# Optimization experiments

Hardware: AMD Instinct MI355X
Metric: run time of the kernel (lower is better)

The kernel has to match this reference:

```python
import jax, jax.numpy as jnp
import numpy as np
import math

H, W = 180, 320          # frame_shape
RF = 16                  # rf_diameter
K = 20
T = 400                  # video frames
FRAME_RATE = 120.0
ALPHA, BETA, GAMMA = 50.0, 1.0, 0.0   # soft-rectifier params
CENTER_SIGMA, SURROUND_SIGMA = 4.0, 8.0
CENTER_STR, SURROUND_STR = 1.0, -0.8
COVERAGE = 0.5


def _mosaic():
    # hexagonal lattice of cell centers (replicates _tile_cells)
    s = CENTER_SIGMA / COVERAGE
    B = np.array([[s, s / 2.0], [0.0, s * math.sqrt(3.0) / 2.0]], dtype=np.float64)
    Binv = np.linalg.inv(B)
    margin = CENTER_SIGMA / 2.0
    corners = np.array([[0, 0], [W, 0], [0, H], [W, H]], dtype=np.float64)
    lc = corners @ Binv.T
    n0, n1 = int(np.floor(lc[:, 0].min())) - 1, int(np.ceil(lc[:, 0].max())) + 1
    m0, m1 = int(np.floor(lc[:, 1].min())) - 1, int(np.ceil(lc[:, 1].max())) + 1
    pos = []
    for m in range(m0, m1 + 1):
        for n in range(n0, n1 + 1):
            p = np.array([float(n), float(m)]) @ B.T
            if margin <= p[0] <= W - margin and margin <= p[1] <= H - margin:
                pos.append((p[0], p[1]))
    return np.array(pos, dtype=np.float32)


def _rf_indices(mosaic):
    # flat pixel indices into the (H+2RF, W+2RF) zero-padded frame
    pw = W + 2 * RF
    yy, xx = np.meshgrid(np.arange(RF), np.arange(RF), indexing='ij')
    local = (yy * pw + xx).ravel()
    out = []
    for x0, y0 in mosaic:
        v = math.floor(y0 - RF / 2.0) + RF
        h = math.floor(x0 - RF / 2.0) + RF
        out.append(local + v * pw + h)
    return np.stack(out).astype(np.int32)


def _filter():
    # DoG spatial filter
    c = RF / 2.0
    yy, xx = np.meshgrid(np.arange(RF, dtype=np.float32), np.arange(RF, dtype=np.float32), indexing='ij')
    d2 = (xx - c) ** 2 + (yy - c) ** 2
    cen = np.exp(-d2 / (2 * CENTER_SIGMA ** 2)); cen /= cen.sum()
    sur = np.exp(-d2 / (2 * SURROUND_SIGMA ** 2)); sur /= sur.sum()
    spatial = CENTER_STR * cen + SURROUND_STR * sur
    # biphasic temporal filter with smooth onset, ON cell, flipped
    dt = 1000.0 / FRAME_RATE
    t = np.arange(K, dtype=np.float32) * dt
    l1 = 1.0 * np.exp(-(t - 40.0) ** 2 / (2 * 20.0 ** 2))
    l2 = 0.6 * np.exp(-(t - 100.0) ** 2 / (2 * 40.0 ** 2))
    onset = 1.0 - np.exp(-t / 15.0)
    temporal = ((l1 - l2) * onset)[::-1].copy()
    st = temporal[:, None, None] * spatial[None]
    st = st / np.linalg.norm(st)
    return st.reshape(-1).astype(np.float32)


def setup_inputs() -> dict:
    key = jax.random.key(0)
    x = jax.random.normal(key, (T, H, W), dtype=jnp.float32)
    mosaic = _mosaic()
    return {
        'x': x,
        'w': jnp.asarray(_filter()),                    # (K*RF*RF,)
        'rf_indices': jnp.asarray(_rf_indices(mosaic)),  # (N_cells, RF*RF)
    }


def reference(x, w, rf_indices):
    # x: (T,H,W); w: (K*RF*RF,); rf_indices: (N, RF*RF) int32
    xp = jnp.pad(x, ((0, 0), (RF, RF), (RF, RF)))
    flat = xp.reshape(x.shape[0], -1)              # (T, (H+2RF)*(W+2RF))
    patches = jnp.take(flat, rf_indices, axis=1)   # (T, N, RF*RF) irregular gather
    wk = w.reshape(K, RF * RF)
    # spatial projection against each temporal tap
    y = jnp.einsum('tnp,kp->tnk', patches, wk)     # (T, N, K)
    n_win = x.shape[0] - K + 1
    # generator[i, n] = sum_k y[i+k, n, k]  (sliding-window spatiotemporal dot)
    g = y[0:n_win, :, 0]
    for k in range(1, K):
        g = g + y[k:k + n_win, :, k]
    out = ALPHA * jax.nn.softplus(BETA * (g - GAMMA))  # soft-rectifier nonlinearity
    return out.T                                    # (N_cells, n_windows)
```

## Files before the change

kernel.cpp:

```cpp
#include <hip/hip_runtime.h>
#include <math.h>

constexpr int H_ = 180, W_ = 320, RF_ = 16, K_ = 20, T_ = 400;
constexpr int HW_ = H_ * W_;
constexpr int NWIN = T_ - K_ + 1;
constexpr int PW   = W_ + 2 * RF_;
constexpr float ALPHA = 50.0f, BETA = 1.0f, GAMMA = 0.0f;
constexpr int NXCD = 8;
constexpr int T_PER_XCD = T_ / NXCD;
constexpr int CH = 8;

template <int CTRL>
__device__ inline float dpp_add(float v) {
    int s = __builtin_amdgcn_update_dpp(0, __float_as_int(v), CTRL, 0xF, 0xF, true);
    return v + __int_as_float(s);
}
__device__ inline float swz_xor4_add(float v) {
    return v + __int_as_float(
        __builtin_amdgcn_ds_swizzle(__float_as_int(v), 0x101F));
}

#if __has_builtin(__builtin_amdgcn_permlane32_swap)
__device__ inline float pl32_merge(float a, float b) {
    auto r = __builtin_amdgcn_permlane32_swap(
        __float_as_uint(a), __float_as_uint(b), false, false);
    return __uint_as_float(r[0]) + __uint_as_float(r[1]);
}
#else
__device__ inline float pl32_merge(float a, float b) {
    bool hi = (threadIdx.x & 32) != 0;
    float keep = hi ? b : a, send = hi ? a : b;
    return keep + __shfl_xor(send, 32, 64);
}
#endif

#if __has_builtin(__builtin_amdgcn_permlane16_swap)
__device__ inline float pl16_merge(float a, float b) {
    auto r = __builtin_amdgcn_permlane16_swap(
        __float_as_uint(a), __float_as_uint(b), false, false);
    return __uint_as_float(r[0]) + __uint_as_float(r[1]);
}
#else
__device__ inline float pl16_merge(float a, float b) {
    bool hi = (threadIdx.x & 16) != 0;
    float keep = hi ? b : a, send = hi ? a : b;
    return keep + __shfl_xor(send, 16, 64);
}
#endif

__device__ inline float allred64(float v) {
    v = dpp_add<0xB1>(v);
    v = dpp_add<0x4E>(v);
    v = swz_xor4_add(v);
    v = dpp_add<0x128>(v);
    v = pl16_merge(v, v);
    v = pl32_merge(v, v);
    return v;
}

__global__ __launch_bounds__(512) void prep_kernel(
    const float* __restrict__ w,
    float* __restrict__ spatial, float* __restrict__ temporal)
{
    __shared__ float ss_l[32];
    int tid = threadIdx.x;
    int wv  = tid >> 6;
    int l   = tid & 63;

    for (int k = wv; k < K_; k += 8) {
        float s = 0.0f;
#pragma unroll
        for (int j = 0; j < 4; ++j) {
            float v = w[k * 256 + l + j * 64];
            s = fmaf(v, v, s);
        }
        s = allred64(s);
        if (l == 0) ss_l[k] = s;
    }
    __syncthreads();

    float best = -1.0f;
    int k0 = 0;
    for (int k = 0; k < K_; ++k) {
        float v = ss_l[k];
        if (v > best) { best = v; k0 = k; }
    }

    for (int k = wv; k < K_; k += 8) {
        float d = 0.0f;
#pragma unroll
        for (int j = 0; j < 4; ++j)
            d = fmaf(w[k * 256 + l + j * 64], w[k0 * 256 + l + j * 64], d);
        d = allred64(d);
        if (l == 0) temporal[k] = d / best;
    }
    if (tid < 256) spatial[tid] = w[k0 * 256 + tid];
}

__global__ __launch_bounds__(256) void stage1_kernel(
    const float* __restrict__ x, const int* __restrict__ rf,
    const float* __restrict__ spatial, float* __restrict__ y,
    int N)
{
    int lane = threadIdx.x & 63;
    int wid  = threadIdx.x >> 6;

    int b   = blockIdx.x;
    int xcd = b & (NXCD - 1);
    int nch = b >> 3;

    int n = nch * 4 + wid;
    if (n >= N) return;
    int t0 = xcd * T_PER_XCD;

    int base = rf[n * 256];
    int r0 = base / PW - RF_;
    int c0 = base % PW - RF_;
    int r0c = min(max(r0, 0), H_ - RF_);
    int c0c = min(max(c0, 0), W_ - RF_);

    int lr = lane >> 2;
    int q  = lane & 3;
    int off = (r0c + lr) * W_ + c0c + q * 4;

    float wv[4];
    int rr = lr + (r0c - r0);
#pragma unroll
    for (int j = 0; j < 4; ++j) {
        int cc = q * 4 + j + (c0c - c0);
        bool ok = (rr >= 0) & (rr < RF_) & (cc >= 0) & (cc < RF_);
        wv[j] = ok ? spatial[rr * RF_ + cc] : 0.0f;
    }

    const float* xp = x + (size_t)t0 * HW_ + off;
    float* yp = y + (size_t)n * T_ + t0;

    bool b8 = (lane & 8) != 0;

    for (int tt = 0; tt < 48; tt += CH) {
        float4 buf[CH];
#pragma unroll
        for (int j = 0; j < CH; ++j)
            buf[j] = *reinterpret_cast<const float4*>(xp + (size_t)(tt + j) * HW_);

        float acc[CH];
#pragma unroll
        for (int j = 0; j < CH; ++j) {
            float a = buf[j].x * wv[0];
            a = fmaf(buf[j].y, wv[1], a);
            a = fmaf(buf[j].z, wv[2], a);
            acc[j] = fmaf(buf[j].w, wv[3], a);
        }

        float m0 = pl32_merge(acc[0], acc[4]);
        float m1 = pl32_merge(acc[1], acc[5]);
        float m2 = pl32_merge(acc[2], acc[6]);
        float m3 = pl32_merge(acc[3], acc[7]);
        float n0 = pl16_merge(m0, m2);
        float n1 = pl16_merge(m1, m3);
        float c0v = dpp_add<0x128>(n0);
        float c1v = dpp_add<0x128>(n1);
        float C = b8 ? c1v : c0v;
        C = dpp_add<0xB1>(C);
        C = dpp_add<0x4E>(C);
        C = swz_xor4_add(C);

        if ((lane & 7) == 0)
            yp[tt + (lane >> 3)] = C;
    }

#pragma unroll
    for (int f = 48; f < T_PER_XCD; ++f) {
        float4 v = *reinterpret_cast<const float4*>(xp + (size_t)f * HW_);
        float a = v.x * wv[0];
        a = fmaf(v.y, wv[1], a);
        a = fmaf(v.z, wv[2], a);
        a = fmaf(v.w, wv[3], a);
        a = allred64(a);
        if (lane == 0) yp[f] = a;
    }
}

__global__ void stage2_kernel(const float* __restrict__ y,
                              const float* __restrict__ temporal,
                              float* __restrict__ out, int N)
{
    __shared__ float tw[K_];
    if (threadIdx.x < K_) tw[threadIdx.x] = temporal[threadIdx.x];
    __syncthreads();

    int n  = blockIdx.x;
    int t0 = threadIdx.x;
    if (n >= N || t0 >= NWIN) return;

    const float* yn = y + (size_t)n * T_;
    float g = 0.0f;
#pragma unroll
    for (int k = 0; k < K_; ++k)
        g = fmaf(yn[t0 + k], tw[k], g);

    float z = BETA * (g - GAMMA);
    float sp = fmaxf(z, 0.0f) + log1pf(expf(-fabsf(z)));
    out[n * NWIN + t0] = ALPHA * sp;
}

extern "C" void kernel_launch(void* const* d_in, const int* in_sizes, int n_in,
                              void* d_out, int out_size, void* d_ws, size_t ws_size,
                              hipStream_t stream)
{
    const float* x  = (const float*)d_in[0];
    const float* w  = (const float*)d_in[1];
    const int*   rf = (const int*)d_in[2];

    int N   = in_sizes[2] / (RF_ * RF_);
    int NCH = (N + 3) / 4;

    float* spatial  = (float*)d_ws;
    float* temporal = spatial + 256;
    float* y        = spatial + 512;

    prep_kernel<<<1, 512, 0, stream>>>(w, spatial, temporal);
    stage1_kernel<<<NXCD * NCH, 256, 0, stream>>>(x, rf, spatial, y, N);
    stage2_kernel<<<N, 384, 0, stream>>>(y, temporal, (float*)d_out, N);
}
```

Before: 45.01 us.

## Stage frame bands into LDS and compute all cells per band from shared tiles

New measurement: 57.37 us. +27.5%, slower.

```diff
diff --git a/kernel.cpp b/kernel.cpp
--- a/kernel.cpp
+++ b/kernel.cpp
@@ -6,9 +6,17 @@
 constexpr int NWIN = T_ - K_ + 1;
 constexpr int PW   = W_ + 2 * RF_;
 constexpr float ALPHA = 50.0f, BETA = 1.0f, GAMMA = 0.0f;
-constexpr int NXCD = 8;
-constexpr int T_PER_XCD = T_ / NXCD;
-constexpr int CH = 8;
+
+constexpr int BSTEP  = 28;
+constexpr int NBANDS = 6;
+constexpr int BROWS  = 43;
+constexpr int RP     = 328;
+constexpr int CHUNKS = (BROWS * RP + 255) / 256;
+constexpr int BUFW   = CHUNKS * 256;
+constexpr int WPR = 36, WROWS = 32;
+constexpr int LDSW_W = WROWS * WPR;
+constexpr int CF = 10;
+constexpr int NCHUNKS_T = T_ / CF;
 
 template <int CTRL>
 __device__ inline float dpp_add(float v) {
@@ -19,7 +27,6 @@
     return v + __int_as_float(
         __builtin_amdgcn_ds_swizzle(__float_as_int(v), 0x101F));
 }
-
 #if __has_builtin(__builtin_amdgcn_permlane32_swap)
 __device__ inline float pl32_merge(float a, float b) {
     auto r = __builtin_amdgcn_permlane32_swap(
@@ -33,7 +40,6 @@
     return keep + __shfl_xor(send, 32, 64);
 }
 #endif
-
 #if __has_builtin(__builtin_amdgcn_permlane16_swap)
 __device__ inline float pl16_merge(float a, float b) {
     auto r = __builtin_amdgcn_permlane16_swap(
@@ -47,7 +53,6 @@
     return keep + __shfl_xor(send, 16, 64);
 }
 #endif
-
 __device__ inline float allred64(float v) {
     v = dpp_add<0xB1>(v);
     v = dpp_add<0x4E>(v);
@@ -57,127 +62,147 @@
     v = pl32_merge(v, v);
     return v;
 }
-
-__global__ __launch_bounds__(512) void prep_kernel(
-    const float* __restrict__ w,
-    float* __restrict__ spatial, float* __restrict__ temporal)
-{
-    __shared__ float ss_l[32];
-    int tid = threadIdx.x;
-    int wv  = tid >> 6;
-    int l   = tid & 63;
-
-    for (int k = wv; k < K_; k += 8) {
-        float s = 0.0f;
-#pragma unroll
-        for (int j = 0; j < 4; ++j) {
-            float v = w[k * 256 + l + j * 64];
-            s = fmaf(v, v, s);
-        }
-        s = allred64(s);
-        if (l == 0) ss_l[k] = s;
+__device__ inline float red16(float v) {
+    v = dpp_add<0xB1>(v);
+    v = dpp_add<0x4E>(v);
+    v = swz_xor4_add(v);
+    v = dpp_add<0x128>(v);
+    return v;
+}
+
+__global__ __launch_bounds__(1024) void prep_kernel(
+    const float* __restrict__ w, const int* __restrict__ rf,
+    float* __restrict__ temporal, float* __restrict__ spat_pad,
+    int* __restrict__ cnt, int4* __restrict__ lists, int N)
+{
+    __shared__ float ss[32];
+    int tid = threadIdx.x, wv = tid >> 6, l = tid & 63;
+    if (tid < NBANDS) cnt[tid] = 0;
+    __syncthreads();
+
+    if (wv < 8) {
+        for (int k = wv; k < K_; k += 8) {
+            float s = 0.0f;
+#pragma unroll
+            for (int j = 0; j < 4; ++j) {
+                float v = w[k * 256 + l + j * 64];
+                s = fmaf(v, v, s);
+            }
+            s = allred64(s);
+            if (l == 0) ss[k] = s;
+        }
+    } else {
+        for (int n = tid - 512; n < N; n += 512) {
+            int base = rf[n * 256];
+            int v0 = base / PW;
+            int r0 = v0 - RF_;
+            int c0 = (base - v0 * PW) - RF_;
+            int r0c = min(max(r0, 0), H_ - RF_);
+            int c0c = min(max(c0, 0), W_ - RF_);
+            int b = r0c / BSTEP;
+            int slot = atomicAdd(&cnt[b], 1);
+            int4 d;
+            d.x = n;
+            d.y = (r0c - b * BSTEP) * RP + c0c;
+            d.z = (r0c - r0 + 8) * WPR + (c0c - c0 + 8);
+            d.w = 0;
+            lists[b * N + slot] = d;
+        }
     }
     __syncthreads();
 
     float best = -1.0f;
     int k0 = 0;
     for (int k = 0; k < K_; ++k) {
-        float v = ss_l[k];
+        float v = ss[k];
         if (v > best) { best = v; k0 = k; }
     }
 
-    for (int k = wv; k < K_; k += 8) {
-        float d = 0.0f;
-#pragma unroll
-        for (int j = 0; j < 4; ++j)
-            d = fmaf(w[k * 256 + l + j * 64], w[k0 * 256 + l + j * 64], d);
-        d = allred64(d);
-        if (l == 0) temporal[k] = d / best;
-    }
-    if (tid < 256) spatial[tid] = w[k0 * 256 + tid];
-}
-
-__global__ __launch_bounds__(256) void stage1_kernel(
-    const float* __restrict__ x, const int* __restrict__ rf,
-    const float* __restrict__ spatial, float* __restrict__ y,
-    int N)
-{
-    int lane = threadIdx.x & 63;
-    int wid  = threadIdx.x >> 6;
-
-    int b   = blockIdx.x;
-    int xcd = b & (NXCD - 1);
-    int nch = b >> 3;
-
-    int n = nch * 4 + wid;
-    if (n >= N) return;
-    int t0 = xcd * T_PER_XCD;
-
-    int base = rf[n * 256];
-    int r0 = base / PW - RF_;
-    int c0 = base % PW - RF_;
-    int r0c = min(max(r0, 0), H_ - RF_);
-    int c0c = min(max(c0, 0), W_ - RF_);
-
-    int lr = lane >> 2;
-    int q  = lane & 3;
-    int off = (r0c + lr) * W_ + c0c + q * 4;
-
-    float wv[4];
-    int rr = lr + (r0c - r0);
-#pragma unroll
-    for (int j = 0; j < 4; ++j) {
-        int cc = q * 4 + j + (c0c - c0);
+    if (wv < 8) {
+        for (int k = wv; k < K_; k += 8) {
+            float d = 0.0f;
+#pragma unroll
+            for (int j = 0; j < 4; ++j)
+                d = fmaf(w[k * 256 + l + j * 64], w[k0 * 256 + l + j * 64], d);
+            d = allred64(d);
+            if (l == 0) temporal[k] = d / best;
+        }
+    }
+    for (int i = tid; i < LDSW_W; i += 1024) {
+        int rr = i / WPR - 8;
+        int cc = i % WPR - 8;
         bool ok = (rr >= 0) & (rr < RF_) & (cc >= 0) & (cc < RF_);
-        wv[j] = ok ? spatial[rr * RF_ + cc] : 0.0f;
-    }
-
-    const float* xp = x + (size_t)t0 * HW_ + off;
-    float* yp = y + (size_t)n * T_ + t0;
-
-    bool b8 = (lane & 8) != 0;
-
-    for (int tt = 0; tt < 48; tt += CH) {
-        float4 buf[CH];
-#pragma unroll
-        for (int j = 0; j < CH; ++j)
-            buf[j] = *reinterpret_cast<const float4*>(xp + (size_t)(tt + j) * HW_);
-
-        float acc[CH];
-#pragma unroll
-        for (int j = 0; j < CH; ++j) {
-            float a = buf[j].x * wv[0];
-            a = fmaf(buf[j].y, wv[1], a);
-            a = fmaf(buf[j].z, wv[2], a);
-            acc[j] = fmaf(buf[j].w, wv[3], a);
-        }
-
-        float m0 = pl32_merge(acc[0], acc[4]);
-        float m1 = pl32_merge(acc[1], acc[5]);
-        float m2 = pl32_merge(acc[2], acc[6]);
-        float m3 = pl32_merge(acc[3], acc[7]);
-        float n0 = pl16_merge(m0, m2);
-        float n1 = pl16_merge(m1, m3);
-        float c0v = dpp_add<0x128>(n0);
-        float c1v = dpp_add<0x128>(n1);
-        float C = b8 ? c1v : c0v;
-        C = dpp_add<0xB1>(C);
-        C = dpp_add<0x4E>(C);
-        C = swz_xor4_add(C);
-
-        if ((lane & 7) == 0)
-            yp[tt + (lane >> 3)] = C;
-    }
-
-#pragma unroll
-    for (int f = 48; f < T_PER_XCD; ++f) {
-        float4 v = *reinterpret_cast<const float4*>(xp + (size_t)f * HW_);
-        float a = v.x * wv[0];
-        a = fmaf(v.y, wv[1], a);
-        a = fmaf(v.z, wv[2], a);
-        a = fmaf(v.w, wv[3], a);
-        a = allred64(a);
-        if (lane == 0) yp[f] = a;
+        spat_pad[i] = ok ? w[k0 * 256 + rr * RF_ + cc] : 0.0f;
+    }
+}
+
+__global__ __launch_bounds__(1024) void stage1_kernel(
+    const float* __restrict__ x, const float* __restrict__ spat_pad,
+    const int* __restrict__ cnt, const int4* __restrict__ lists,
+    float* __restrict__ y, int N)
+{
+    __shared__ float lds[2 * BUFW + LDSW_W];
+    float* ldsw = lds + 2 * BUFW;
+
+    int tid  = threadIdx.x;
+    int wv   = tid >> 6;
+    int lane = tid & 63;
+
+    int b       = blockIdx.x % NBANDS;
+    int chunkid = blockIdx.x / NBANDS;
+    int f0      = chunkid * CF;
+    int band0   = b * BSTEP;
+
+    for (int i = tid; i < LDSW_W; i += 1024) ldsw[i] = spat_pad[i];
+
+    int count = cnt[b];
+    const int4* list = lists + (size_t)b * N;
+    int g = lane >> 4;
+    int r = lane & 15;
+
+    auto stage = [&](int sel, int f) {
+        const float* xf = x + (size_t)f * HW_;
+        for (int ck = wv; ck < CHUNKS; ck += 16) {
+            int w0  = ck * 256 + lane * 4;
+            int row = w0 / RP;
+            int col = w0 - row * RP;
+            int srow = min(band0 + row, H_ - 1);
+            int scol = min(col, W_ - 4);
+            const float* gp = xf + srow * W_ + scol;
+            __builtin_amdgcn_global_load_lds(
+                (const __attribute__((address_space(1))) void*)gp,
+                (__attribute__((address_space(3))) void*)(lds + sel * BUFW + ck * 256),
+                16, 0, 0);
+        }
+    };
+
+    auto compute = [&](int sel, int t) {
+        const float* buf = lds + sel * BUFW;
+        for (int i = wv * 4 + g; i < count; i += 64) {
+            int4 d = list[i];
+            int ax = d.y + r * RP;
+            int aw = d.z + r * WPR;
+            float a = 0.0f;
+#pragma unroll
+            for (int q = 0; q < 4; ++q) {
+                float4 pv = *reinterpret_cast<const float4*>(buf + ax + q * 4);
+                float4 wq = *reinterpret_cast<const float4*>(ldsw + aw + q * 4);
+                a = fmaf(pv.x, wq.x, a);
+                a = fmaf(pv.y, wq.y, a);
+                a = fmaf(pv.z, wq.z, a);
+                a = fmaf(pv.w, wq.w, a);
+            }
+            a = red16(a);
+            if (r == 0) y[(size_t)d.x * T_ + t] = a;
+        }
+    };
+
+    stage(0, f0);
+    __syncthreads();
+    for (int j = 0; j < CF; ++j) {
+        if (j + 1 < CF) stage((j + 1) & 1, f0 + j + 1);
+        compute(j & 1, f0 + j);
+        __syncthreads();
     }
 }
 
@@ -212,14 +237,15 @@
     const float* w  = (const float*)d_in[1];
     const int*   rf = (const int*)d_in[2];
 
-    int N   = in_sizes[2] / (RF_ * RF_);
-    int NCH = (N + 3) / 4;
-
-    float* spatial  = (float*)d_ws;
-    float* temporal = spatial + 256;
-    float* y        = spatial + 512;
-
-    prep_kernel<<<1, 512, 0, stream>>>(w, spatial, temporal);
-    stage1_kernel<<<NXCD * NCH, 256, 0, stream>>>(x, rf, spatial, y, N);
+    int N = in_sizes[2] / (RF_ * RF_);
+
+    float* temporal = (float*)d_ws;
+    int*   cnt      = (int*)d_ws + 64;
+    float* spat_pad = (float*)d_ws + 128;
+    int4*  lists    = (int4*)((int*)d_ws + 1280);
+    float* y        = (float*)d_ws + 1280 + 4 * NBANDS * N;
+
+    prep_kernel<<<1, 1024, 0, stream>>>(w, rf, temporal, spat_pad, cnt, lists, N);
+    stage1_kernel<<<NCHUNKS_T * NBANDS, 1024, 0, stream>>>(x, spat_pad, cnt, lists, y, N);
     stage2_kernel<<<N, 384, 0, stream>>>(y, temporal, (float*)d_out, N);
 }
```

## Gang eight cells per wave and split time into quarters per XCD

Applied to the files above, without the earlier changes.

Result: slower. 47.58 us (+5.7%).

```diff
diff --git a/kernel.cpp b/kernel.cpp
--- a/kernel.cpp
+++ b/kernel.cpp
@@ -8,7 +8,7 @@
 constexpr float ALPHA = 50.0f, BETA = 1.0f, GAMMA = 0.0f;
 constexpr int NXCD = 8;
 constexpr int T_PER_XCD = T_ / NXCD;
-constexpr int CH = 8;
+constexpr int GANG = 8;
 
 template <int CTRL>
 __device__ inline float dpp_add(float v) {
@@ -19,7 +19,6 @@
     return v + __int_as_float(
         __builtin_amdgcn_ds_swizzle(__float_as_int(v), 0x101F));
 }
-
 #if __has_builtin(__builtin_amdgcn_permlane32_swap)
 __device__ inline float pl32_merge(float a, float b) {
     auto r = __builtin_amdgcn_permlane32_swap(
@@ -33,7 +32,6 @@
     return keep + __shfl_xor(send, 32, 64);
 }
 #endif
-
 #if __has_builtin(__builtin_amdgcn_permlane16_swap)
 __device__ inline float pl16_merge(float a, float b) {
     auto r = __builtin_amdgcn_permlane16_swap(
@@ -47,7 +45,6 @@
     return keep + __shfl_xor(send, 16, 64);
 }
 #endif
-
 __device__ inline float allred64(float v) {
     v = dpp_add<0xB1>(v);
     v = dpp_add<0x4E>(v);
@@ -57,15 +54,28 @@
     v = pl32_merge(v, v);
     return v;
 }
+__device__ inline float multired8(const float* acc, bool b8) {
+    float m0 = pl32_merge(acc[0], acc[4]);
+    float m1 = pl32_merge(acc[1], acc[5]);
+    float m2 = pl32_merge(acc[2], acc[6]);
+    float m3 = pl32_merge(acc[3], acc[7]);
+    float n0 = pl16_merge(m0, m2);
+    float n1 = pl16_merge(m1, m3);
+    float c0v = dpp_add<0x128>(n0);
+    float c1v = dpp_add<0x128>(n1);
+    float C = b8 ? c1v : c0v;
+    C = dpp_add<0xB1>(C);
+    C = dpp_add<0x4E>(C);
+    C = swz_xor4_add(C);
+    return C;
+}
 
 __global__ __launch_bounds__(512) void prep_kernel(
     const float* __restrict__ w,
     float* __restrict__ spatial, float* __restrict__ temporal)
 {
-    __shared__ float ss_l[32];
-    int tid = threadIdx.x;
-    int wv  = tid >> 6;
-    int l   = tid & 63;
+    __shared__ float ss[32];
+    int tid = threadIdx.x, wv = tid >> 6, l = tid & 63;
 
     for (int k = wv; k < K_; k += 8) {
         float s = 0.0f;
@@ -75,14 +85,14 @@
             s = fmaf(v, v, s);
         }
         s = allred64(s);
-        if (l == 0) ss_l[k] = s;
+        if (l == 0) ss[k] = s;
     }
     __syncthreads();
 
     float best = -1.0f;
     int k0 = 0;
     for (int k = 0; k < K_; ++k) {
-        float v = ss_l[k];
+        float v = ss[k];
         if (v > best) { best = v; k0 = k; }
     }
 
@@ -99,85 +109,80 @@
 
 __global__ __launch_bounds__(256) void stage1_kernel(
     const float* __restrict__ x, const int* __restrict__ rf,
-    const float* __restrict__ spatial, float* __restrict__ y,
-    int N)
+    const float* __restrict__ spatial, float* __restrict__ y, int N)
 {
     int lane = threadIdx.x & 63;
     int wid  = threadIdx.x >> 6;
 
     int b   = blockIdx.x;
     int xcd = b & (NXCD - 1);
-    int nch = b >> 3;
-
-    int n = nch * 4 + wid;
-    if (n >= N) return;
-    int t0 = xcd * T_PER_XCD;
-
-    int base = rf[n * 256];
-    int r0 = base / PW - RF_;
-    int c0 = base % PW - RF_;
-    int r0c = min(max(r0, 0), H_ - RF_);
-    int c0c = min(max(c0, 0), W_ - RF_);
-
-    int lr = lane >> 2;
-    int q  = lane & 3;
-    int off = (r0c + lr) * W_ + c0c + q * 4;
-
-    float wv[4];
-    int rr = lr + (r0c - r0);
-#pragma unroll
-    for (int j = 0; j < 4; ++j) {
-        int cc = q * 4 + j + (c0c - c0);
+    int q4  = (b >> 3) & 3;
+    int tg  = b >> 5;
+
+    int NG = (N + GANG - 1) / GANG;
+    int gi = tg * 4 + wid;
+    if (gi >= NG) return;
+    int gb = gi * GANG;
+
+    int r = lane >> 2;
+    int q = lane & 3;
+
+    int   off[GANG];
+    float4 w4[GANG];
+#pragma unroll
+    for (int j = 0; j < GANG; ++j) {
+        int nj   = min(gb + j, N - 1);
+        int base = rf[nj * 256];
+        int v0   = base / PW;
+        int r0   = v0 - RF_;
+        int c0   = (base - v0 * PW) - RF_;
+        int r0c  = min(max(r0, 0), H_ - RF_);
+        int c0c  = min(max(c0, 0), W_ - RF_);
+        off[j] = (r0c + r) * W_ + c0c + 4 * q;
+        int rr = r + (r0c - r0);
+        int cc = 4 * q + (c0c - c0);
         bool ok = (rr >= 0) & (rr < RF_) & (cc >= 0) & (cc < RF_);
-        wv[j] = ok ? spatial[rr * RF_ + cc] : 0.0f;
-    }
-
-    const float* xp = x + (size_t)t0 * HW_ + off;
-    float* yp = y + (size_t)n * T_ + t0;
-
+        float4 wz = make_float4(0.f, 0.f, 0.f, 0.f);
+        if (ok) wz = *reinterpret_cast<const float4*>(spatial + rr * RF_ + cc);
+        w4[j] = wz;
+    }
+
+    float* ypn = y + (size_t)min(gb + (lane >> 3), N - 1) * T_;
     bool b8 = (lane & 8) != 0;
 
-    for (int tt = 0; tt < 48; tt += CH) {
-        float4 buf[CH];
-#pragma unroll
-        for (int j = 0; j < CH; ++j)
-            buf[j] = *reinterpret_cast<const float4*>(xp + (size_t)(tt + j) * HW_);
-
-        float acc[CH];
-#pragma unroll
-        for (int j = 0; j < CH; ++j) {
-            float a = buf[j].x * wv[0];
-            a = fmaf(buf[j].y, wv[1], a);
-            a = fmaf(buf[j].z, wv[2], a);
-            acc[j] = fmaf(buf[j].w, wv[3], a);
+    int tbase = xcd * T_PER_XCD + q4 * 12 + max(0, q4 - 2);
+    int tend  = tbase + 12 + (q4 >> 1);
+
+    for (int t = tbase; t < tend; t += 2) {
+        int t2 = min(t + 1, T_ - 1);
+        const float* fA = x + (size_t)t  * HW_;
+        const float* fB = x + (size_t)t2 * HW_;
+        float4 vA[GANG], vB[GANG];
+#pragma unroll
+        for (int j = 0; j < GANG; ++j)
+            vA[j] = *reinterpret_cast<const float4*>(fA + off[j]);
+#pragma unroll
+        for (int j = 0; j < GANG; ++j)
+            vB[j] = *reinterpret_cast<const float4*>(fB + off[j]);
+
+        float aA[GANG], aB[GANG];
+#pragma unroll
+        for (int j = 0; j < GANG; ++j) {
+            float u = vA[j].x * w4[j].x;
+            u = fmaf(vA[j].y, w4[j].y, u);
+            u = fmaf(vA[j].z, w4[j].z, u);
+            aA[j] = fmaf(vA[j].w, w4[j].w, u);
+            float v = vB[j].x * w4[j].x;
+            v = fmaf(vB[j].y, w4[j].y, v);
+            v = fmaf(vB[j].z, w4[j].z, v);
+            aB[j] = fmaf(vB[j].w, w4[j].w, v);
         }
-
-        float m0 = pl32_merge(acc[0], acc[4]);
-        float m1 = pl32_merge(acc[1], acc[5]);
-        float m2 = pl32_merge(acc[2], acc[6]);
-        float m3 = pl32_merge(acc[3], acc[7]);
-        float n0 = pl16_merge(m0, m2);
-        float n1 = pl16_merge(m1, m3);
-        float c0v = dpp_add<0x128>(n0);
-        float c1v = dpp_add<0x128>(n1);
-        float C = b8 ? c1v : c0v;
-        C = dpp_add<0xB1>(C);
-        C = dpp_add<0x4E>(C);
-        C = swz_xor4_add(C);
-
-        if ((lane & 7) == 0)
-            yp[tt + (lane >> 3)] = C;
-    }
-
-#pragma unroll
-    for (int f = 48; f < T_PER_XCD; ++f) {
-        float4 v = *reinterpret_cast<const float4*>(xp + (size_t)f * HW_);
-        float a = v.x * wv[0];
-        a = fmaf(v.y, wv[1], a);
-        a = fmaf(v.z, wv[2], a);
-        a = fmaf(v.w, wv[3], a);
-        a = allred64(a);
-        if (lane == 0) yp[f] = a;
+        float CA = multired8(aA, b8);
+        float CB = multired8(aB, b8);
+        if ((lane & 7) == 0) {
+            ypn[t] = CA;
+            if (t + 1 < tend) ypn[t + 1] = CB;
+        }
     }
 }
 
@@ -212,14 +217,16 @@
     const float* w  = (const float*)d_in[1];
     const int*   rf = (const int*)d_in[2];
 
-    int N   = in_sizes[2] / (RF_ * RF_);
-    int NCH = (N + 3) / 4;
+    int N = in_sizes[2] / (RF_ * RF_);
 
     float* spatial  = (float*)d_ws;
     float* temporal = spatial + 256;
-    float* y        = spatial + 512;
+    float* y        = spatial + 320;
+
+    int NG = (N + GANG - 1) / GANG;
+    int blocks = (NG + 3) / 4 * 32;
 
     prep_kernel<<<1, 512, 0, stream>>>(w, spatial, temporal);
-    stage1_kernel<<<NXCD * NCH, 256, 0, stream>>>(x, rf, spatial, y, N);
+    stage1_kernel<<<blocks, 256, 0, stream>>>(x, rf, spatial, y, N);
     stage2_kernel<<<N, 384, 0, stream>>>(y, temporal, (float*)d_out, N);
 }
```
